# Performance work log

Measured on AMD Instinct MI355X. Metric: run time of the kernel, lower is better.

Reference implementation:

```python
import jax, jax.numpy as jnp
import numpy as np

NEG_INF = jnp.float32(-jnp.inf)


def setup_inputs() -> dict:
    key = jax.random.key(0)
    k1, k2, k3, k4 = jax.random.split(key, 4)
    B, T, E = 8, 2048, 1024
    H_DK = 1024  # dk * num_heads
    scale = 1.0 / np.sqrt(E)
    x = jax.random.normal(k1, (B, T, E), dtype=jnp.float32)
    Wq = jax.random.normal(k2, (E, H_DK), dtype=jnp.float32) * scale
    Wk = jax.random.normal(k3, (E, H_DK), dtype=jnp.float32) * scale
    Wv = jax.random.normal(k4, (E, H_DK), dtype=jnp.float32) * scale
    return {"x": x, "Wq": Wq, "Wk": Wk, "Wv": Wv, "dk": 64}


def reference(x, Wq, Wk, Wv, dk):
    # x: [B, T, E]; Wq/Wk/Wv: [E, H*dk] (heads never split in original module)
    Q = jnp.einsum("bte,ed->btd", x, Wq)
    K = jnp.einsum("bte,ed->btd", x, Wk)
    V = jnp.einsum("bte,ed->btd", x, Wv)
    energy = jnp.einsum("bqd,bkd->bqk", Q, K)  # [B, T, T]
    B, T, _ = energy.shape
    # padding mask derived from first query row: lengths[b] = #nonzero of energy[b,0,:]
    lengths = jnp.sum(energy[:, 0] != 0, axis=-1)  # [B]
    j = jnp.arange(T)
    pad_mask = j[None, :] >= lengths[:, None]          # [B, T] -> key positions masked
    causal_mask = j[None, :] > j[:, None]              # [T, T]
    mask = pad_mask[:, None, :] | causal_mask[None, :, :]  # [B, T, T]
    energy = jnp.where(mask, NEG_INF, energy)
    score = jax.nn.softmax(energy / jnp.sqrt(jnp.float32(dk)), axis=-1)
    return jnp.einsum("bqk,bkd->bqd", score, V)
```

## Files before the change

kernel.cpp:

```cpp
#include <hip/hip_runtime.h>

#define DEV __device__ __forceinline__

using f32x4 = __attribute__((ext_vector_type(4))) float;
using f16x8 = __attribute__((ext_vector_type(8))) _Float16;
using f16x4 = __attribute__((ext_vector_type(4))) _Float16;

constexpr int Bc = 8, Tc = 2048, Ec = 1024, Hc = 1024;
constexpr int Mc = Bc * Tc;
constexpr int SLOTA = 128 * 32;
constexpr int SLOTB = 256 * 32;

DEV f32x4 mfma16(f16x8 a, f16x8 b, f32x4 c) {
    return __builtin_amdgcn_mfma_f32_16x16x32_f16(a, b, c, 0, 0, 0);
}
DEV unsigned short f16bits(float f) { return __builtin_bit_cast(unsigned short, (_Float16)f); }
DEV float f16val(unsigned short u) { return (float)__builtin_bit_cast(_Float16, u); }

DEV void gload16(const _Float16* g, _Float16* l) {
    __builtin_amdgcn_global_load_lds(
        (const __attribute__((address_space(1))) unsigned int*)g,
        (__attribute__((address_space(3))) unsigned int*)l, 16, 0, 0);
}

DEV int swz_off(int R, int lk) {
    return ((R >> 1) << 6) + ((((((R & 1) << 2) | lk) ^ ((R >> 1) & 7))) << 3);
}

__global__ __launch_bounds__(256) void prep_x(const float* __restrict__ x,
                                              _Float16* __restrict__ xf, int n) {
    int i = (blockIdx.x * 256 + threadIdx.x) * 4;
    if (i >= n) return;
    f32x4 v = *reinterpret_cast<const f32x4*>(x + i);
    f16x4 h;
#pragma unroll
    for (int j = 0; j < 4; j++) h[j] = (_Float16)v[j];
    *reinterpret_cast<f16x4*>(xf + i) = h;
}

__global__ __launch_bounds__(256) void prep_w(const float* __restrict__ wq,
                                              const float* __restrict__ wk,
                                              const float* __restrict__ wv,
                                              _Float16* __restrict__ wall) {
    __shared__ float tile[32][33];
    const int z = blockIdx.z;
    const float* src = (z == 0) ? wq : (z == 1) ? wk : wv;
    _Float16* dh = wall + (size_t)z * 1024 * Ec;
    const int n0 = blockIdx.x * 32, e0 = blockIdx.y * 32;
    const int tx = threadIdx.x & 31, ty = threadIdx.x >> 5;
#pragma unroll
    for (int j = 0; j < 32; j += 8)
        tile[ty + j][tx] = src[(size_t)(e0 + ty + j) * Hc + n0 + tx];
    __syncthreads();
#pragma unroll
    for (int j = 0; j < 32; j += 8)
        dh[(size_t)(n0 + ty + j) * Ec + e0 + tx] = (_Float16)tile[tx][ty + j];
}

template <int EPI>
DEV void gemm_body(int bx, int mt, int z,
                   const _Float16* __restrict__ Ah, const _Float16* __restrict__ Bh,
                   void* __restrict__ out0, void* __restrict__ out2,
                   const int* __restrict__ dkp,
                   int lda, int ldb, size_t aBS, size_t bBS, size_t oBS, int nkt,
                   _Float16* sAb, _Float16* sBb) {
    if (EPI == 3) nkt = ((mt >> 1) + 1) * 8;

    Ah += (size_t)z * aBS;
    Bh += (size_t)z * bBS;

    const float scale = (EPI == 2) ? (1.0f / sqrtf((float)*dkp)) : 1.0f;

    const int tid = threadIdx.x;
    const int wave = tid >> 6, lane = tid & 63;
    const int lr = lane & 15, lk = lane >> 4;
    const int wn = wave;
    const int m0 = mt * 128, n0 = bx * 256;

    const int so = (lane & 7) ^ (lane >> 3);
    const int strow = 2 * (lane >> 3) + (so >> 2);
    const int stcol = (so & 3) * 8;
    const size_t aoff0 = (size_t)(m0 + (wave * 2 + 0) * 16 + strow) * lda + stcol;
    const size_t aoff1 = (size_t)(m0 + (wave * 2 + 1) * 16 + strow) * lda + stcol;
    size_t boff[4];
#pragma unroll
    for (int l = 0; l < 4; l++)
        boff[l] = (size_t)(n0 + (wave * 4 + l) * 16 + strow) * ldb + stcol;
    const int lda0 = (wave * 2 + 0) * 512, lda1 = (wave * 2 + 1) * 512;

    auto stage = [&](int sv, int slot) {
        const int kk = sv * 32;
        _Float16* dA = sAb + slot * SLOTA;
        _Float16* dB = sBb + slot * SLOTB;
        gload16(Ah + aoff0 + kk, dA + lda0);
        gload16(Ah + aoff1 + kk, dA + lda1);
#pragma unroll
        for (int l = 0; l < 4; l++)
            gload16(Bh + boff[l] + kk, dB + (wave * 4 + l) * 512);
    };

    f32x4 acc[8][4] = {};

    stage(0, 0);
    stage(1, 1);
    asm volatile("s_waitcnt vmcnt(6)" ::: "memory");
    __builtin_amdgcn_s_barrier();

    int rP = 0;
    for (int P = 0; P < nkt; ++P) {
        const _Float16* cA = sAb + rP * SLOTA;
        const _Float16* cB = sBb + rP * SLOTB;
        f16x8 af[8], bfr[4];

#pragma unroll
        for (int nj = 0; nj < 4; nj++)
            bfr[nj] = *reinterpret_cast<const f16x8*>(
                &cB[swz_off(wn * 64 + nj * 16 + lr, lk)]);
#pragma unroll
        for (int mi = 0; mi < 8; mi++)
            af[mi] = *reinterpret_cast<const f16x8*>(
                &cA[swz_off(mi * 16 + lr, lk)]);

        int rs = rP + 2; if (rs >= 3) rs -= 3;
        if (P + 2 < nkt) stage(P + 2, rs);

        __builtin_amdgcn_s_setprio(1);
#pragma unroll
        for (int mi = 0; mi < 8; mi++)
#pragma unroll
            for (int nj = 0; nj < 4; nj++)
                acc[mi][nj] = mfma16(af[mi], bfr[nj], acc[mi][nj]);
        __builtin_amdgcn_s_setprio(0);

        if (P + 2 < nkt) {
            asm volatile("s_waitcnt vmcnt(6)" ::: "memory");
            __builtin_amdgcn_s_barrier();
        } else if (P + 1 < nkt) {
            asm volatile("s_waitcnt vmcnt(0)" ::: "memory");
            __builtin_amdgcn_s_barrier();
        }
        if (++rP == 3) rP = 0;
    }

#pragma unroll
    for (int mi = 0; mi < 8; mi++)
#pragma unroll
        for (int nj = 0; nj < 4; nj++) {
            const int gn = n0 + wn * 64 + nj * 16 + lr;
            if (EPI == 1) {
                const int gm0 = m0 + mi * 16 + lk * 4;
                const int bb = gm0 >> 11, t = gm0 & (Tc - 1);
                f16x4 pk;
#pragma unroll
                for (int r = 0; r < 4; r++) pk[r] = (_Float16)acc[mi][nj][r];
                *reinterpret_cast<f16x4*>(
                    &((_Float16*)out0)[((size_t)(bb * Hc + gn)) * Tc + t]) = pk;
            } else if (EPI == 0) {
                _Float16* od = (gn < 1024) ? (_Float16*)out0 : (_Float16*)out2;
                const int cc = gn & 1023;
#pragma unroll
                for (int r = 0; r < 4; r++) {
                    const int gm = m0 + mi * 16 + lk * 4 + r;
                    od[(size_t)gm * Hc + cc] = (_Float16)acc[mi][nj][r];
                }
            } else {
#pragma unroll
                for (int r = 0; r < 4; r++) {
                    const int gm = m0 + mi * 16 + lk * 4 + r;
                    const float v = acc[mi][nj][r];
                    if (EPI == 2) {
                        const float e = (gn > gm) ? -INFINITY : v * scale;
                        ((unsigned short*)out0)[(size_t)z * oBS + (size_t)gm * Tc + gn] =
                            f16bits(e);
                    } else {
                        ((float*)out0)[(size_t)z * oBS + (size_t)gm * Hc + gn] = v;
                    }
                }
            }
        }
}

__global__ __launch_bounds__(256, 2) void k_qkv(
        const _Float16* __restrict__ Xf, const _Float16* __restrict__ Wall,
        _Float16* __restrict__ Qf, _Float16* __restrict__ Kf,
        _Float16* __restrict__ Vt, const int* __restrict__ dkp) {
    __shared__ _Float16 sA[3][SLOTA];
    __shared__ _Float16 sB[3][SLOTB];
    const int i = blockIdx.x;
    if (i < 1024) {
        const int w = (i & 7) * 128 + (i >> 3);
        const int mt = w >> 3, bx = w & 7;
        gemm_body<0>(bx, mt, 0, Xf, Wall, Qf, Kf, dkp,
                     Ec, Ec, 0, 0, 0, 32, sA[0], sB[0]);
    } else {
        const int j = i - 1024;
        gemm_body<1>(j & 3, j >> 2, 0, Xf, Wall + (size_t)2048 * Ec,
                     Vt, nullptr, dkp, Ec, Ec, 0, 0, 0, 32, sA[0], sB[0]);
    }
}

__global__ __launch_bounds__(256, 2) void k_energy(
        const _Float16* __restrict__ Qf, const _Float16* __restrict__ Kf,
        unsigned short* __restrict__ S, const int* __restrict__ dkp) {
    __shared__ _Float16 sA[3][SLOTA];
    __shared__ _Float16 sB[3][SLOTB];
    const int i = blockIdx.x;
    const int b = i / 72;
    int t = i - b * 72;
    int qb = 0;
    while (t >= (qb >> 1) + 1) { t -= (qb >> 1) + 1; qb++; }
    gemm_body<2>(t, qb, b, Qf, Kf, S, nullptr, dkp,
                 Hc, Hc, (size_t)Tc * Hc, (size_t)Tc * Hc, (size_t)Tc * Tc, 32,
                 sA[0], sB[0]);
}

__global__ __launch_bounds__(256, 2) void k_pv(
        const _Float16* __restrict__ S, const _Float16* __restrict__ Vt,
        float* __restrict__ out, const int* __restrict__ dkp) {
    __shared__ _Float16 sA[3][SLOTA];
    __shared__ _Float16 sB[3][SLOTB];
    const int lin = blockIdx.x;
    const int b = lin >> 6;
    const int r = lin & 63;
    const int bx = r & 3, half = (r >> 2) & 1, pp = r >> 3;
    const int qb = half ? 15 - pp : pp;
    gemm_body<3>(bx, qb, b, S, Vt, out, nullptr, dkp,
                 Tc, Tc, (size_t)Tc * Tc, (size_t)Hc * Tc, (size_t)Tc * Hc, 0,
                 sA[0], sB[0]);
}

__global__ __launch_bounds__(256) void softmax_k(unsigned short* __restrict__ S) {
    const int q = blockIdx.x & (Tc - 1);
    const int b = blockIdx.x >> 11;
    const int tid = threadIdx.x;
    const int c0 = tid * 8;
    const int limit = ((q >> 8) + 1) << 8;
    const bool active = c0 < limit;
    unsigned short* row = S + ((size_t)b * Tc + q) * Tc;

    float v[8];
    if (active) {
        uint4 raw = *reinterpret_cast<const uint4*>(row + c0);
        unsigned u[4] = {raw.x, raw.y, raw.z, raw.w};
#pragma unroll
        for (int p = 0; p < 4; p++) {
            v[2 * p]     = f16val((unsigned short)(u[p] & 0xFFFFu));
            v[2 * p + 1] = f16val((unsigned short)(u[p] >> 16));
        }
#pragma unroll
        for (int i = 0; i < 8; i++)
            if (c0 + i > q) v[i] = -INFINITY;
    } else {
#pragma unroll
        for (int i = 0; i < 8; i++) v[i] = -INFINITY;
    }

    float m = v[0];
#pragma unroll
    for (int i = 1; i < 8; i++) m = fmaxf(m, v[i]);
#pragma unroll
    for (int off = 1; off < 64; off <<= 1) m = fmaxf(m, __shfl_xor(m, off));
    __shared__ float red[4];
    if ((tid & 63) == 0) red[tid >> 6] = m;
    __syncthreads();
    m = fmaxf(fmaxf(red[0], red[1]), fmaxf(red[2], red[3]));

    float e[8], s = 0.f;
#pragma unroll
    for (int i = 0; i < 8; i++) {
        e[i] = __expf(v[i] - m);
        s += e[i];
    }
#pragma unroll
    for (int off = 1; off < 64; off <<= 1) s += __shfl_xor(s, off);
    __syncthreads();
    if ((tid & 63) == 0) red[tid >> 6] = s;
    __syncthreads();
    s = red[0] + red[1] + red[2] + red[3];
    const float inv = 1.0f / s;

    if (active) {
        unsigned o[4];
#pragma unroll
        for (int p = 0; p < 4; p++) {
            unsigned short a = f16bits(e[2 * p] * inv);
            unsigned short bb = f16bits(e[2 * p + 1] * inv);
            o[p] = (unsigned)a | ((unsigned)bb << 16);
        }
        uint4 w; w.x = o[0]; w.y = o[1]; w.z = o[2]; w.w = o[3];
        *reinterpret_cast<uint4*>(row + c0) = w;
    }
}

extern "C" void kernel_launch(void* const* d_in, const int* in_sizes, int n_in,
                              void* d_out, int out_size, void* d_ws, size_t ws_size,
                              hipStream_t stream) {
    const float* x  = (const float*)d_in[0];
    const float* Wq = (const float*)d_in[1];
    const float* Wk = (const float*)d_in[2];
    const float* Wv = (const float*)d_in[3];
    const int*   dk = (const int*)d_in[4];
    float* out = (float*)d_out;
    char* ws = (char*)d_ws;

    const size_t SZ_XE = (size_t)Mc * Ec * 2;
    const size_t SZ_W  = (size_t)Ec * Hc * 2;

    size_t o = 0;
    auto nxt = [&](size_t bytes) { void* p = ws + o; o += bytes; return p; };
    _Float16* Qf   = (_Float16*)nxt(SZ_XE);
    _Float16* Kf   = (_Float16*)nxt(SZ_XE);
    _Float16* Vt   = (_Float16*)nxt(SZ_XE);
    _Float16* Xf   = (_Float16*)nxt(SZ_XE);
    _Float16* Wall = (_Float16*)nxt(3 * SZ_W);
    unsigned short* S = (unsigned short*)Xf;
    (void)ws_size; (void)in_sizes; (void)n_in; (void)out_size;

    prep_x<<<(Mc * Ec / 4 + 255) / 256, 256, 0, stream>>>(x, Xf, Mc * Ec);
    prep_w<<<dim3(32, 32, 3), 256, 0, stream>>>(Wq, Wk, Wv, Wall);

    k_qkv<<<1536, 256, 0, stream>>>(Xf, Wall, Qf, Kf, Vt, dk);

    k_energy<<<576, 256, 0, stream>>>(Qf, Kf, (unsigned short*)S, dk);

    softmax_k<<<Bc * Tc, 256, 0, stream>>>((unsigned short*)S);

    k_pv<<<512, 256, 0, stream>>>((const _Float16*)S, Vt, out, dk);
}
```

Baseline: 295.0 us.

## Use 256x256 tiles with 8 waves for the QKV projection GEMM

Adds a new 8-wave (512-thread) GEMM body with a 256x256 output tile and uses it for the QKV projection kernel, halving the grid to 768 blocks. Each wave now loads two A and two B 16-row strips per stage, so LDS staging per block covers both operands at 256 rows. This is meant to raise operand reuse and arithmetic intensity per byte loaded from global memory and LDS. In exchange, LDS per block grows to about 96KB, which may limit occupancy to one block per CU, and the smaller grid may give coarser load balance.

```diff
diff --git a/kernel.cpp b/kernel.cpp
--- a/kernel.cpp
+++ b/kernel.cpp
@@ -8,8 +8,8 @@
 
 constexpr int Bc = 8, Tc = 2048, Ec = 1024, Hc = 1024;
 constexpr int Mc = Bc * Tc;
+constexpr int SLOT  = 256 * 32;
 constexpr int SLOTA = 128 * 32;
-constexpr int SLOTB = 256 * 32;
 
 DEV f32x4 mfma16(f16x8 a, f16x8 b, f32x4 c) {
     return __builtin_amdgcn_mfma_f32_16x16x32_f16(a, b, c, 0, 0, 0);
@@ -58,12 +58,109 @@
 }
 
 template <int EPI>
-DEV void gemm_body(int bx, int mt, int z,
-                   const _Float16* __restrict__ Ah, const _Float16* __restrict__ Bh,
-                   void* __restrict__ out0, void* __restrict__ out2,
-                   const int* __restrict__ dkp,
-                   int lda, int ldb, size_t aBS, size_t bBS, size_t oBS, int nkt,
-                   _Float16* sAb, _Float16* sBb) {
+DEV void gemm8_body(int bx, int by, int z,
+                    const _Float16* __restrict__ Ah, const _Float16* __restrict__ Bh,
+                    void* __restrict__ out0, void* __restrict__ out2,
+                    int lda, int ldb, int nkt,
+                    _Float16* sAb, _Float16* sBb) {
+    const int tid = threadIdx.x;
+    const int wave = tid >> 6, lane = tid & 63;
+    const int lr = lane & 15, lk = lane >> 4;
+    const int wm = wave >> 2, wn = wave & 3;
+    const int m0 = by * 256, n0 = bx * 256;
+
+    const int so = (lane & 7) ^ (lane >> 3);
+    const int strow = 2 * (lane >> 3) + (so >> 2);
+    const int stcol = (so & 3) * 8;
+    const size_t aoff0 = (size_t)(m0 + (wave * 2 + 0) * 16 + strow) * lda + stcol;
+    const size_t aoff1 = (size_t)(m0 + (wave * 2 + 1) * 16 + strow) * lda + stcol;
+    const size_t boff0 = (size_t)(n0 + (wave * 2 + 0) * 16 + strow) * ldb + stcol;
+    const size_t boff1 = (size_t)(n0 + (wave * 2 + 1) * 16 + strow) * ldb + stcol;
+    const int ld0 = (wave * 2 + 0) * 512, ld1 = (wave * 2 + 1) * 512;
+
+    auto stage = [&](int sv, int slot) {
+        const int kk = sv * 32;
+        _Float16* dA = sAb + slot * SLOT;
+        _Float16* dB = sBb + slot * SLOT;
+        gload16(Ah + aoff0 + kk, dA + ld0);
+        gload16(Ah + aoff1 + kk, dA + ld1);
+        gload16(Bh + boff0 + kk, dB + ld0);
+        gload16(Bh + boff1 + kk, dB + ld1);
+    };
+
+    f32x4 acc[8][4] = {};
+
+    stage(0, 0);
+    stage(1, 1);
+    asm volatile("s_waitcnt vmcnt(4)" ::: "memory");
+    __builtin_amdgcn_s_barrier();
+
+    int rP = 0;
+    for (int P = 0; P < nkt; ++P) {
+        const _Float16* cA = sAb + rP * SLOT;
+        const _Float16* cB = sBb + rP * SLOT;
+        f16x8 af[8], bfr[4];
+#pragma unroll
+        for (int nj = 0; nj < 4; nj++)
+            bfr[nj] = *reinterpret_cast<const f16x8*>(
+                &cB[swz_off(wn * 64 + nj * 16 + lr, lk)]);
+#pragma unroll
+        for (int mi = 0; mi < 8; mi++)
+            af[mi] = *reinterpret_cast<const f16x8*>(
+                &cA[swz_off(wm * 128 + mi * 16 + lr, lk)]);
+
+        int rs = rP + 2; if (rs >= 3) rs -= 3;
+        if (P + 2 < nkt) stage(P + 2, rs);
+
+        __builtin_amdgcn_s_setprio(1);
+#pragma unroll
+        for (int mi = 0; mi < 8; mi++)
+#pragma unroll
+            for (int nj = 0; nj < 4; nj++)
+                acc[mi][nj] = mfma16(af[mi], bfr[nj], acc[mi][nj]);
+        __builtin_amdgcn_s_setprio(0);
+
+        if (P + 2 < nkt) {
+            asm volatile("s_waitcnt vmcnt(4)" ::: "memory");
+            __builtin_amdgcn_s_barrier();
+        } else if (P + 1 < nkt) {
+            asm volatile("s_waitcnt vmcnt(0)" ::: "memory");
+            __builtin_amdgcn_s_barrier();
+        }
+        if (++rP == 3) rP = 0;
+    }
+
+#pragma unroll
+    for (int mi = 0; mi < 8; mi++)
+#pragma unroll
+        for (int nj = 0; nj < 4; nj++) {
+            const int gn = n0 + wn * 64 + nj * 16 + lr;
+            if (EPI == 1) {
+                const int gm0 = m0 + wm * 128 + mi * 16 + lk * 4;
+                const int bb = gm0 >> 11, t = gm0 & (Tc - 1);
+                f16x4 pk;
+#pragma unroll
+                for (int r = 0; r < 4; r++) pk[r] = (_Float16)acc[mi][nj][r];
+                *reinterpret_cast<f16x4*>(
+                    &((_Float16*)out0)[((size_t)(bb * Hc + gn)) * Tc + t]) = pk;
+            } else {
+                _Float16* od = (gn < 1024) ? (_Float16*)out0 : (_Float16*)out2;
+                const int cc = gn & 1023;
+#pragma unroll
+                for (int r = 0; r < 4; r++) {
+                    const int gm = m0 + wm * 128 + mi * 16 + lk * 4 + r;
+                    od[(size_t)gm * Hc + cc] = (_Float16)acc[mi][nj][r];
+                }
+            }
+        }
+}
+
+template <int EPI>
+DEV void gemm4_body(int bx, int mt, int z,
+                    const _Float16* __restrict__ Ah, const _Float16* __restrict__ Bh,
+                    void* __restrict__ out0, const int* __restrict__ dkp,
+                    int lda, int ldb, size_t aBS, size_t bBS, size_t oBS, int nkt,
+                    _Float16* sAb, _Float16* sBb) {
     if (EPI == 3) nkt = ((mt >> 1) + 1) * 8;
 
     Ah += (size_t)z * aBS;
@@ -91,7 +188,7 @@
     auto stage = [&](int sv, int slot) {
         const int kk = sv * 32;
         _Float16* dA = sAb + slot * SLOTA;
-        _Float16* dB = sBb + slot * SLOTB;
+        _Float16* dB = sBb + slot * SLOT;
         gload16(Ah + aoff0 + kk, dA + lda0);
         gload16(Ah + aoff1 + kk, dA + lda1);
 #pragma unroll
@@ -109,9 +206,8 @@
     int rP = 0;
     for (int P = 0; P < nkt; ++P) {
         const _Float16* cA = sAb + rP * SLOTA;
-        const _Float16* cB = sBb + rP * SLOTB;
+        const _Float16* cB = sBb + rP * SLOT;
         f16x8 af[8], bfr[4];
-
 #pragma unroll
         for (int nj = 0; nj < 4; nj++)
             bfr[nj] = *reinterpret_cast<const f16x8*>(
@@ -147,86 +243,68 @@
 #pragma unroll
         for (int nj = 0; nj < 4; nj++) {
             const int gn = n0 + wn * 64 + nj * 16 + lr;
-            if (EPI == 1) {
-                const int gm0 = m0 + mi * 16 + lk * 4;
-                const int bb = gm0 >> 11, t = gm0 & (Tc - 1);
-                f16x4 pk;
-#pragma unroll
-                for (int r = 0; r < 4; r++) pk[r] = (_Float16)acc[mi][nj][r];
-                *reinterpret_cast<f16x4*>(
-                    &((_Float16*)out0)[((size_t)(bb * Hc + gn)) * Tc + t]) = pk;
-            } else if (EPI == 0) {
-                _Float16* od = (gn < 1024) ? (_Float16*)out0 : (_Float16*)out2;
-                const int cc = gn & 1023;
-#pragma unroll
-                for (int r = 0; r < 4; r++) {
-                    const int gm = m0 + mi * 16 + lk * 4 + r;
-                    od[(size_t)gm * Hc + cc] = (_Float16)acc[mi][nj][r];
-                }
-            } else {
-#pragma unroll
-                for (int r = 0; r < 4; r++) {
-                    const int gm = m0 + mi * 16 + lk * 4 + r;
-                    const float v = acc[mi][nj][r];
-                    if (EPI == 2) {
-                        const float e = (gn > gm) ? -INFINITY : v * scale;
-                        ((unsigned short*)out0)[(size_t)z * oBS + (size_t)gm * Tc + gn] =
-                            f16bits(e);
-                    } else {
-                        ((float*)out0)[(size_t)z * oBS + (size_t)gm * Hc + gn] = v;
-                    }
+#pragma unroll
+            for (int r = 0; r < 4; r++) {
+                const int gm = m0 + mi * 16 + lk * 4 + r;
+                const float v = acc[mi][nj][r];
+                if (EPI == 2) {
+                    const float e = (gn > gm) ? -INFINITY : v * scale;
+                    ((unsigned short*)out0)[(size_t)z * oBS + (size_t)gm * Tc + gn] =
+                        f16bits(e);
+                } else {
+                    ((float*)out0)[(size_t)z * oBS + (size_t)gm * Hc + gn] = v;
                 }
             }
         }
 }
 
-__global__ __launch_bounds__(256, 2) void k_qkv(
+__global__ __launch_bounds__(512, 2) void k_qkv(
         const _Float16* __restrict__ Xf, const _Float16* __restrict__ Wall,
         _Float16* __restrict__ Qf, _Float16* __restrict__ Kf,
         _Float16* __restrict__ Vt, const int* __restrict__ dkp) {
-    __shared__ _Float16 sA[3][SLOTA];
-    __shared__ _Float16 sB[3][SLOTB];
+    __shared__ _Float16 sA[3][SLOT];
+    __shared__ _Float16 sB[3][SLOT];
     const int i = blockIdx.x;
-    if (i < 1024) {
-        const int w = (i & 7) * 128 + (i >> 3);
-        const int mt = w >> 3, bx = w & 7;
-        gemm_body<0>(bx, mt, 0, Xf, Wall, Qf, Kf, dkp,
-                     Ec, Ec, 0, 0, 0, 32, sA[0], sB[0]);
+    if (i < 512) {
+        const int w = (i & 7) * 64 + (i >> 3);
+        const int by = w >> 3, bx = w & 7;
+        gemm8_body<0>(bx, by, 0, Xf, Wall, Qf, Kf, Ec, Ec, 32, sA[0], sB[0]);
     } else {
-        const int j = i - 1024;
-        gemm_body<1>(j & 3, j >> 2, 0, Xf, Wall + (size_t)2048 * Ec,
-                     Vt, nullptr, dkp, Ec, Ec, 0, 0, 0, 32, sA[0], sB[0]);
-    }
+        const int j = i - 512;
+        gemm8_body<1>(j & 3, j >> 2, 0, Xf, Wall + (size_t)2048 * Ec,
+                      Vt, nullptr, Ec, Ec, 32, sA[0], sB[0]);
+    }
+    (void)dkp;
 }
 
 __global__ __launch_bounds__(256, 2) void k_energy(
         const _Float16* __restrict__ Qf, const _Float16* __restrict__ Kf,
         unsigned short* __restrict__ S, const int* __restrict__ dkp) {
     __shared__ _Float16 sA[3][SLOTA];
-    __shared__ _Float16 sB[3][SLOTB];
+    __shared__ _Float16 sB[3][SLOT];
     const int i = blockIdx.x;
     const int b = i / 72;
     int t = i - b * 72;
     int qb = 0;
     while (t >= (qb >> 1) + 1) { t -= (qb >> 1) + 1; qb++; }
-    gemm_body<2>(t, qb, b, Qf, Kf, S, nullptr, dkp,
-                 Hc, Hc, (size_t)Tc * Hc, (size_t)Tc * Hc, (size_t)Tc * Tc, 32,
-                 sA[0], sB[0]);
+    gemm4_body<2>(t, qb, b, Qf, Kf, S, dkp,
+                  Hc, Hc, (size_t)Tc * Hc, (size_t)Tc * Hc, (size_t)Tc * Tc, 32,
+                  sA[0], sB[0]);
 }
 
 __global__ __launch_bounds__(256, 2) void k_pv(
         const _Float16* __restrict__ S, const _Float16* __restrict__ Vt,
         float* __restrict__ out, const int* __restrict__ dkp) {
     __shared__ _Float16 sA[3][SLOTA];
-    __shared__ _Float16 sB[3][SLOTB];
+    __shared__ _Float16 sB[3][SLOT];
     const int lin = blockIdx.x;
     const int b = lin >> 6;
     const int r = lin & 63;
     const int bx = r & 3, half = (r >> 2) & 1, pp = r >> 3;
     const int qb = half ? 15 - pp : pp;
-    gemm_body<3>(bx, qb, b, S, Vt, out, nullptr, dkp,
-                 Tc, Tc, (size_t)Tc * Tc, (size_t)Hc * Tc, (size_t)Tc * Hc, 0,
-                 sA[0], sB[0]);
+    gemm4_body<3>(bx, qb, b, S, Vt, out, dkp,
+                  Tc, Tc, (size_t)Tc * Tc, (size_t)Hc * Tc, (size_t)Tc * Hc, 0,
+                  sA[0], sB[0]);
 }
 
 __global__ __launch_bounds__(256) void softmax_k(unsigned short* __restrict__ S) {
@@ -319,7 +397,7 @@
     prep_x<<<(Mc * Ec / 4 + 255) / 256, 256, 0, stream>>>(x, Xf, Mc * Ec);
     prep_w<<<dim3(32, 32, 3), 256, 0, stream>>>(Wq, Wk, Wv, Wall);
 
-    k_qkv<<<1536, 256, 0, stream>>>(Xf, Wall, Qf, Kf, Vt, dk);
+    k_qkv<<<768, 512, 0, stream>>>(Xf, Wall, Qf, Kf, Vt, dk);
 
     k_energy<<<576, 256, 0, stream>>>(Qf, Kf, (unsigned short*)S, dk);
 
```

Measured after the change: 293.6 us. About the same (-0.5%).
